# Kernel tuning notes

Measured on AMD Instinct MI355X. Metric: run time of the kernel, lower is better.

Reference implementation:

```python
import jax, jax.numpy as jnp
import numpy as np

NUM_HEAD = 8


def setup_inputs() -> dict:
    key = jax.random.key(0)
    ks = jax.random.split(key, 9)
    B, C, H, W = 4, 32, 1024, 64  # [batch, dim_input, Input_len, nodes]
    s = 1.0 / np.sqrt(C)
    return {
        "x": jax.random.normal(ks[0], (B, C, H, W), dtype=jnp.float32),
        # 1x1 conv weights stored as [out, in]
        "wq": jax.random.normal(ks[1], (C, C), dtype=jnp.float32) * s,
        "bq": jax.random.normal(ks[2], (C,), dtype=jnp.float32) * 0.01,
        "wk": jax.random.normal(ks[3], (C, C), dtype=jnp.float32) * s,
        "bk": jax.random.normal(ks[4], (C,), dtype=jnp.float32) * 0.01,
        "wv": jax.random.normal(ks[5], (C, C), dtype=jnp.float32) * s,
        "bv": jax.random.normal(ks[6], (C,), dtype=jnp.float32) * 0.01,
        # nn.Linear(num_head, 1): weight [1, num_head], bias [1]
        "w_lin": jax.random.normal(ks[7], (1, NUM_HEAD), dtype=jnp.float32) * (1.0 / np.sqrt(NUM_HEAD)),
        "b_lin": jax.random.normal(ks[8], (1,), dtype=jnp.float32) * 0.01,
    }


def reference(x, wq, bq, wk, bk, wv, bv, w_lin, b_lin):
    # x: [B, C, H, W]; 1x1 conv == channel matmul
    def conv1x1(w, b):
        return jnp.einsum("bchw,oc->bohw", x, w) + b[None, :, None, None]

    # transpose(-3,-1): [B, C, H, W] -> [B, W, H, C]
    q = conv1x1(wq, bq).transpose(0, 3, 2, 1)  # [B, W, H, C]
    k = conv1x1(wk, bk).transpose(0, 3, 2, 1)  # [B, W, H, C]
    v = conv1x1(wv, bv).transpose(0, 3, 2, 1)  # [B, W, H, C]

    H = x.shape[2]
    kd = jnp.sqrt(jnp.float32(H) / NUM_HEAD)
    scores = jnp.einsum("bwhc,bwgc->bwhg", q, k) / kd  # [B, W, H, H]
    attn = jax.nn.softmax(scores, axis=-1)
    line = jnp.einsum("bwhg,bwgc->bwhc", attn, v)  # [B, W, H, C]

    # All num_head heads share weights (dropout=identity at eval), so
    # linear1 over the stacked-head axis == line * sum(w_lin) + b_lin.
    result = line * jnp.sum(w_lin) + b_lin[0]
    # squeeze(-1) then transpose(1,3): [B, W, H, C] -> [B, C, H, W]
    return result.transpose(0, 3, 2, 1)
```

## Files before the change

### kernel.cpp

```cpp
#include <hip/hip_runtime.h>

typedef unsigned short u16;
typedef unsigned int   u32;
typedef __bf16 bf16x8 __attribute__((ext_vector_type(8)));
typedef float  f32x4  __attribute__((ext_vector_type(4)));

#define KSCALE 0.12751743f

__device__ __forceinline__ u32 cvtpk(float lo, float hi) {
    u32 r;
    asm("v_cvt_pk_bf16_f32 %0, %1, %2" : "=v"(r) : "v"(lo), "v"(hi));
    return r;
}

__global__ __launch_bounds__(256, 4) void qkv_proj(
    const float* __restrict__ x,
    const float* __restrict__ wq, const float* __restrict__ bq,
    const float* __restrict__ wk, const float* __restrict__ bk,
    const float* __restrict__ wv, const float* __restrict__ bv,
    u16* __restrict__ Qb, u16* __restrict__ Kb, u16* __restrict__ Vb)
{
    __shared__ __align__(16) u16 sW[3][32][40];
    __shared__ float sB[3][32];
    __shared__ __align__(16) u16 sO[8192];
    const int tid = threadIdx.x;
    const int b  = blockIdx.x >> 8;
    const int h0 = (blockIdx.x & 255) * 4;
    const int wid = tid >> 6, lane = tid & 63;
    const int g = lane >> 4, c = lane & 15;

    {
        const float* Ws[3] = {wq, wk, wv};
#pragma unroll
        for (int m = 0; m < 3; m++) {
            const float sc = (m == 1) ? KSCALE : 1.0f;
            for (int i = tid; i < 512; i += 256) {
                float2 v = ((const float2*)Ws[m])[i];
                int co = i >> 4, cip = i & 15;
                ((u32*)&sW[m][co][0])[cip] = cvtpk(v.x * sc, v.y * sc);
            }
        }
        if (tid < 96) {
            const float* Bs[3] = {bq, bk, bv};
            float v = Bs[tid >> 5][tid & 31];
            if ((tid >> 5) == 1) v *= KSCALE;
            ((float*)sB)[tid] = v;
        }
    }

    bf16x8 xf[4];
    {
        const float* xb = x + (size_t)b * 2097152 + (size_t)h0 * 64 + wid * 64;
#pragma unroll
        for (int pt = 0; pt < 4; pt++) {
            float f[8];
#pragma unroll
            for (int j = 0; j < 8; j++)
                f[j] = xb[(size_t)(8 * g + j) * 65536 + pt * 16 + c];
            uint4 u;
            u.x = cvtpk(f[0], f[1]); u.y = cvtpk(f[2], f[3]);
            u.z = cvtpk(f[4], f[5]); u.w = cvtpk(f[6], f[7]);
            xf[pt] = __builtin_bit_cast(bf16x8, u);
        }
    }
    __syncthreads();

    u16* outs[3] = {Qb, Kb, Vb};
    const f32x4 zz = {0.f, 0.f, 0.f, 0.f};

#pragma unroll
    for (int m = 0; m < 3; m++) {
        bf16x8 wf[2];
        float4 bias[2];
#pragma unroll
        for (int a = 0; a < 2; a++) {
            wf[a] = __builtin_bit_cast(bf16x8,
                *(const uint4*)((const char*)&sW[m][a * 16 + c][0] + g * 16));
            bias[a] = *(const float4*)&sB[m][a * 16 + g * 4];
        }

        f32x4 o[2][4];
#pragma unroll
        for (int a = 0; a < 2; a++)
#pragma unroll
            for (int pt = 0; pt < 4; pt++)
                o[a][pt] = __builtin_amdgcn_mfma_f32_16x16x32_bf16(wf[a], xf[pt], zz, 0, 0, 0);

        if (m) __syncthreads();

#pragma unroll
        for (int a = 0; a < 2; a++)
#pragma unroll
            for (int pt = 0; pt < 4; pt++) {
                int w = pt * 16 + c;
                float v0 = o[a][pt][0] + bias[a].x;
                float v1 = o[a][pt][1] + bias[a].y;
                float v2 = o[a][pt][2] + bias[a].z;
                float v3 = o[a][pt][3] + bias[a].w;
                uint2 st;
                st.x = cvtpk(v0, v1);
                st.y = cvtpk(v2, v3);
                int chunk = (wid * 4 + a * 2 + (g >> 1)) ^ (w & 7);
                *(uint2*)((char*)sO + w * 256 + chunk * 16 + (g & 1) * 8) = st;
            }
        __syncthreads();

        u16* gout = outs[m];
#pragma unroll
        for (int i = 0; i < 4; i++) {
            int L = tid + i * 256;
            int w_ = L >> 4, lc = L & 15;
            uint4 val = *(const uint4*)((const char*)sO + w_ * 256 + ((lc ^ (w_ & 7)) << 4));
            int hh = lc >> 2, sub = lc & 3;
            size_t off;
            if (m == 1) {
                int kv = h0 + hh;
                int q5 = kv & 31;
                int slot = (kv & ~31) | ((q5 & 4) << 2) | ((q5 & 24) >> 1) | (q5 & 3);
                off = (size_t)(b * 64 + w_) * 32768 + slot * 32 + (sub ^ ((slot >> 1) & 3)) * 8;
            } else {
                off = (size_t)(b * 64 + w_) * 32768 + (h0 + hh) * 32 + sub * 8;
            }
            *(uint4*)(gout + off) = val;
        }
    }
}

__global__ __launch_bounds__(1024, 2) void attn(
    const u16* __restrict__ Qb, const u16* __restrict__ Kb,
    const u16* __restrict__ Vb, float* __restrict__ Ow)
{
    __shared__ __align__(16) char sK[65536];
    __shared__ __align__(16) char sV[65536];
    const int tid = threadIdx.x;
    const int p = blockIdx.x;

    {
        const uint4* gK = (const uint4*)(Kb + (size_t)p * 32768);
        uint4* sK4 = (uint4*)sK;
        for (int m = tid; m < 4096; m += 1024)
            sK4[m] = gK[m];
        const uint4* gV = (const uint4*)(Vb + (size_t)p * 32768);
        for (int m = tid; m < 4096; m += 1024) {
            uint4 val = gV[m];
            int kv = m >> 2, c0 = (m & 3) * 8;
            const u16* pv = (const u16*)&val;
#pragma unroll
            for (int k = 0; k < 8; k++) {
                int d = c0 + k;
                int chv = (kv >> 3) ^ (d & 7) ^ ((d >> 3) & 3);
                *(u16*)(sV + d * 2048 + (chv << 4) + (kv & 7) * 2) = pv[k];
            }
        }
    }
    __syncthreads();

    const int wid = tid >> 6, lane = tid & 63;
    const int g = lane >> 4, c = lane & 15;

    bf16x8 qf[4];
    {
        const u16* qbase = Qb + (size_t)p * 32768;
#pragma unroll
        for (int nq = 0; nq < 4; nq++) {
            int row = wid * 64 + nq * 16 + c;
            qf[nq] = __builtin_bit_cast(bf16x8, *(const uint4*)(qbase + row * 32 + g * 8));
        }
    }

    bf16x8 ones;
    {
        uint4 u; u.x = u.y = u.z = u.w = 0x3F803F80u;
        ones = __builtin_bit_cast(bf16x8, u);
    }

    f32x4 o[4][2];
    f32x4 ls[4];
    const f32x4 zz = {0.f, 0.f, 0.f, 0.f};
#pragma unroll
    for (int nq = 0; nq < 4; nq++) { o[nq][0] = zz; o[nq][1] = zz; ls[nq] = zz; }

    for (int j = 0; j < 32; j++) {
        const int kv0 = j * 32;
        const int ra = kv0 + c;
        const int rb = ra + 16;
        bf16x8 k0 = __builtin_bit_cast(bf16x8,
            *(const uint4*)(sK + ra * 64 + ((g ^ ((ra >> 1) & 3)) << 4)));
        bf16x8 k1 = __builtin_bit_cast(bf16x8,
            *(const uint4*)(sK + rb * 64 + ((g ^ ((rb >> 1) & 3)) << 4)));
        const int cb = (kv0 >> 3) + g;
        bf16x8 v0 = __builtin_bit_cast(bf16x8,
            *(const uint4*)(sV + c * 2048 + ((cb ^ (c & 7) ^ ((c >> 3) & 3)) << 4)));
        bf16x8 v1 = __builtin_bit_cast(bf16x8,
            *(const uint4*)(sV + (c + 16) * 2048 + ((cb ^ (c & 7) ^ (((c + 16) >> 3) & 3)) << 4)));

        f32x4 sA[4], sB_[4];
#pragma unroll
        for (int nq = 0; nq < 4; nq++) {
            sA[nq]  = __builtin_amdgcn_mfma_f32_16x16x32_bf16(k0, qf[nq], zz, 0, 0, 0);
            sB_[nq] = __builtin_amdgcn_mfma_f32_16x16x32_bf16(k1, qf[nq], zz, 0, 0, 0);
        }
        __builtin_amdgcn_sched_barrier(0);

        bf16x8 pf[4];
#pragma unroll
        for (int nq = 0; nq < 4; nq++) {
            float p0[4], p1[4];
#pragma unroll
            for (int r = 0; r < 4; r++) {
                p0[r] = __builtin_amdgcn_exp2f(sA[nq][r]);
                p1[r] = __builtin_amdgcn_exp2f(sB_[nq][r]);
            }
            uint4 pw;
            pw.x = cvtpk(p0[0], p0[1]);
            pw.y = cvtpk(p0[2], p0[3]);
            pw.z = cvtpk(p1[0], p1[1]);
            pw.w = cvtpk(p1[2], p1[3]);
            pf[nq] = __builtin_bit_cast(bf16x8, pw);
        }
        __builtin_amdgcn_sched_barrier(0);

#pragma unroll
        for (int nq = 0; nq < 4; nq++) {
            o[nq][0] = __builtin_amdgcn_mfma_f32_16x16x32_bf16(v0, pf[nq], o[nq][0], 0, 0, 0);
            o[nq][1] = __builtin_amdgcn_mfma_f32_16x16x32_bf16(v1, pf[nq], o[nq][1], 0, 0, 0);
            ls[nq]   = __builtin_amdgcn_mfma_f32_16x16x32_bf16(ones, pf[nq], ls[nq], 0, 0, 0);
        }
    }

#pragma unroll
    for (int nq = 0; nq < 4; nq++) {
        const float inv = 1.0f / ls[nq][0];
        const int hq = wid * 64 + nq * 16 + c;
        float* dst = Ow + (size_t)p * 32768 + hq;
#pragma unroll
        for (int t = 0; t < 2; t++)
#pragma unroll
            for (int r = 0; r < 4; r++) {
                int d = t * 16 + g * 4 + r;
                dst[(size_t)d * 1024] = o[nq][t][r] * inv;
            }
    }
}

__global__ __launch_bounds__(256) void finalize_tr(
    const float* __restrict__ Ow, const float* __restrict__ w_lin,
    const float* __restrict__ b_lin, float* __restrict__ out)
{
    __shared__ float tile[64][65];
    const int tid = threadIdx.x;
    const int bi = blockIdx.x;
    const int b = bi >> 9, d = (bi >> 4) & 31, ht = bi & 15;
    const int h0 = ht * 64;

    float slin = 0.f;
#pragma unroll
    for (int i = 0; i < 8; i++) slin += w_lin[i];
    const float bl = b_lin[0];

    const int w = tid >> 2, part = tid & 3;
    const float4* src = (const float4*)(Ow + (((size_t)b * 64 + w) * 32 + d) * 1024 + h0 + part * 16);
#pragma unroll
    for (int i = 0; i < 4; i++) {
        float4 v = src[i];
        int hh = part * 16 + i * 4;
        tile[w][hh + 0] = v.x; tile[w][hh + 1] = v.y;
        tile[w][hh + 2] = v.z; tile[w][hh + 3] = v.w;
    }
    __syncthreads();

    const int ww = tid & 63, hb = tid >> 6;
    const size_t obase = ((size_t)b * 32 + d) * 1024 + h0;
#pragma unroll
    for (int k = 0; k < 16; k++) {
        int hh = k * 4 + hb;
        out[(obase + hh) * 64 + ww] = tile[ww][hh] * slin + bl;
    }
}

extern "C" void kernel_launch(void* const* d_in, const int* in_sizes, int n_in,
                              void* d_out, int out_size, void* d_ws, size_t ws_size,
                              hipStream_t stream)
{
    const float* x  = (const float*)d_in[0];
    const float* wq = (const float*)d_in[1];
    const float* bq = (const float*)d_in[2];
    const float* wk = (const float*)d_in[3];
    const float* bk = (const float*)d_in[4];
    const float* wv = (const float*)d_in[5];
    const float* bv = (const float*)d_in[6];
    const float* wl = (const float*)d_in[7];
    const float* bl = (const float*)d_in[8];
    float* out = (float*)d_out;

    char* ws = (char*)d_ws;
    u16*   Qb = (u16*)(ws);
    u16*   Kb = (u16*)(ws + (16u << 20));
    u16*   Vb = (u16*)(ws + (32u << 20));
    float* Ow = (float*)(ws + (48u << 20));

    qkv_proj<<<1024, 256, 0, stream>>>(x, wq, bq, wk, bk, wv, bv, Qb, Kb, Vb);
    attn<<<256, 1024, 0, stream>>>(Qb, Kb, Vb, Ow);
    finalize_tr<<<2048, 256, 0, stream>>>(Ow, wl, bl, out);
}
```

Measured before the change: 73.65 us.

## Software-pipeline QK^T MFMAs with softmax and store attention output as bf16

```diff
diff --git a/kernel.cpp b/kernel.cpp
--- a/kernel.cpp
+++ b/kernel.cpp
@@ -11,6 +11,9 @@
     u32 r;
     asm("v_cvt_pk_bf16_f32 %0, %1, %2" : "=v"(r) : "v"(lo), "v"(hi));
     return r;
+}
+__device__ __forceinline__ float bf2f(u32 lo16) {
+    return __builtin_bit_cast(float, lo16 << 16);
 }
 
 __global__ __launch_bounds__(256, 4) void qkv_proj(
@@ -128,7 +131,7 @@
 
 __global__ __launch_bounds__(1024, 2) void attn(
     const u16* __restrict__ Qb, const u16* __restrict__ Kb,
-    const u16* __restrict__ Vb, float* __restrict__ Ow)
+    const u16* __restrict__ Vb, u16* __restrict__ Ow)
 {
     __shared__ __align__(16) char sK[65536];
     __shared__ __align__(16) char sV[65536];
@@ -180,31 +183,48 @@
 #pragma unroll
     for (int nq = 0; nq < 4; nq++) { o[nq][0] = zz; o[nq][1] = zz; ls[nq] = zz; }
 
-    for (int j = 0; j < 32; j++) {
-        const int kv0 = j * 32;
-        const int ra = kv0 + c;
-        const int rb = ra + 16;
-        bf16x8 k0 = __builtin_bit_cast(bf16x8,
-            *(const uint4*)(sK + ra * 64 + ((g ^ ((ra >> 1) & 3)) << 4)));
-        bf16x8 k1 = __builtin_bit_cast(bf16x8,
-            *(const uint4*)(sK + rb * 64 + ((g ^ ((rb >> 1) & 3)) << 4)));
-        const int cb = (kv0 >> 3) + g;
-        bf16x8 v0 = __builtin_bit_cast(bf16x8,
-            *(const uint4*)(sV + c * 2048 + ((cb ^ (c & 7) ^ ((c >> 3) & 3)) << 4)));
-        bf16x8 v1 = __builtin_bit_cast(bf16x8,
-            *(const uint4*)(sV + (c + 16) * 2048 + ((cb ^ (c & 7) ^ (((c + 16) >> 3) & 3)) << 4)));
-
-        f32x4 sA[4], sB_[4];
+#define LOADKV(j_, K0, K1, V0, V1)                                              \
+    {                                                                           \
+        const int kv0_ = (j_) * 32;                                             \
+        const int ra_ = kv0_ + c;                                               \
+        const int rb_ = ra_ + 16;                                               \
+        K0 = __builtin_bit_cast(bf16x8,                                         \
+            *(const uint4*)(sK + ra_ * 64 + ((g ^ ((ra_ >> 1) & 3)) << 4)));    \
+        K1 = __builtin_bit_cast(bf16x8,                                         \
+            *(const uint4*)(sK + rb_ * 64 + ((g ^ ((rb_ >> 1) & 3)) << 4)));    \
+        const int cb_ = (kv0_ >> 3) + g;                                        \
+        V0 = __builtin_bit_cast(bf16x8,                                         \
+            *(const uint4*)(sV + c * 2048 + ((cb_ ^ (c & 7) ^ ((c >> 3) & 3)) << 4)));              \
+        V1 = __builtin_bit_cast(bf16x8,                                         \
+            *(const uint4*)(sV + (c + 16) * 2048 + ((cb_ ^ (c & 7) ^ (((c + 16) >> 3) & 3)) << 4)));\
+    }
+
+    f32x4 sA[4], sB_[4];
+    bf16x8 v0c, v1c;
+    {
+        bf16x8 k0, k1;
+        LOADKV(0, k0, k1, v0c, v1c);
 #pragma unroll
         for (int nq = 0; nq < 4; nq++) {
             sA[nq]  = __builtin_amdgcn_mfma_f32_16x16x32_bf16(k0, qf[nq], zz, 0, 0, 0);
             sB_[nq] = __builtin_amdgcn_mfma_f32_16x16x32_bf16(k1, qf[nq], zz, 0, 0, 0);
         }
-        __builtin_amdgcn_sched_barrier(0);
+    }
+
+    for (int j = 0; j < 32; j++) {
+        bf16x8 k0n, k1n, v0n, v1n;
+        f32x4 sAn[4] = {zz, zz, zz, zz};
+        f32x4 sBn[4] = {zz, zz, zz, zz};
+        const bool more = (j < 31);
+        if (more) LOADKV(j + 1, k0n, k1n, v0n, v1n);
 
         bf16x8 pf[4];
 #pragma unroll
         for (int nq = 0; nq < 4; nq++) {
+            if (more) {
+                sAn[nq] = __builtin_amdgcn_mfma_f32_16x16x32_bf16(k0n, qf[nq], zz, 0, 0, 0);
+                sBn[nq] = __builtin_amdgcn_mfma_f32_16x16x32_bf16(k1n, qf[nq], zz, 0, 0, 0);
+            }
             float p0[4], p1[4];
 #pragma unroll
             for (int r = 0; r < 4; r++) {
@@ -220,31 +240,39 @@
         }
         __builtin_amdgcn_sched_barrier(0);
 
+        __builtin_amdgcn_s_setprio(1);
 #pragma unroll
         for (int nq = 0; nq < 4; nq++) {
-            o[nq][0] = __builtin_amdgcn_mfma_f32_16x16x32_bf16(v0, pf[nq], o[nq][0], 0, 0, 0);
-            o[nq][1] = __builtin_amdgcn_mfma_f32_16x16x32_bf16(v1, pf[nq], o[nq][1], 0, 0, 0);
+            o[nq][0] = __builtin_amdgcn_mfma_f32_16x16x32_bf16(v0c, pf[nq], o[nq][0], 0, 0, 0);
+            o[nq][1] = __builtin_amdgcn_mfma_f32_16x16x32_bf16(v1c, pf[nq], o[nq][1], 0, 0, 0);
             ls[nq]   = __builtin_amdgcn_mfma_f32_16x16x32_bf16(ones, pf[nq], ls[nq], 0, 0, 0);
         }
-    }
+        __builtin_amdgcn_s_setprio(0);
+
+#pragma unroll
+        for (int nq = 0; nq < 4; nq++) { sA[nq] = sAn[nq]; sB_[nq] = sBn[nq]; }
+        v0c = v0n; v1c = v1n;
+    }
+#undef LOADKV
 
 #pragma unroll
     for (int nq = 0; nq < 4; nq++) {
         const float inv = 1.0f / ls[nq][0];
         const int hq = wid * 64 + nq * 16 + c;
-        float* dst = Ow + (size_t)p * 32768 + hq;
+        u16* dst = Ow + (size_t)p * 32768 + hq;
 #pragma unroll
         for (int t = 0; t < 2; t++)
 #pragma unroll
             for (int r = 0; r < 4; r++) {
                 int d = t * 16 + g * 4 + r;
-                dst[(size_t)d * 1024] = o[nq][t][r] * inv;
+                float v = o[nq][t][r] * inv;
+                dst[(size_t)d * 1024] = (u16)cvtpk(v, v);
             }
     }
 }
 
 __global__ __launch_bounds__(256) void finalize_tr(
-    const float* __restrict__ Ow, const float* __restrict__ w_lin,
+    const u16* __restrict__ Ow, const float* __restrict__ w_lin,
     const float* __restrict__ b_lin, float* __restrict__ out)
 {
     __shared__ float tile[64][65];
@@ -259,13 +287,17 @@
     const float bl = b_lin[0];
 
     const int w = tid >> 2, part = tid & 3;
-    const float4* src = (const float4*)(Ow + (((size_t)b * 64 + w) * 32 + d) * 1024 + h0 + part * 16);
-#pragma unroll
-    for (int i = 0; i < 4; i++) {
-        float4 v = src[i];
-        int hh = part * 16 + i * 4;
-        tile[w][hh + 0] = v.x; tile[w][hh + 1] = v.y;
-        tile[w][hh + 2] = v.z; tile[w][hh + 3] = v.w;
+    const u16* src = Ow + (((size_t)b * 64 + w) * 32 + d) * 1024 + h0 + part * 16;
+#pragma unroll
+    for (int i = 0; i < 2; i++) {
+        uint4 v = ((const uint4*)src)[i];
+        int hh = part * 16 + i * 8;
+        u32 a[4] = {v.x, v.y, v.z, v.w};
+#pragma unroll
+        for (int e = 0; e < 4; e++) {
+            tile[w][hh + 2 * e]     = bf2f(a[e] & 0xFFFFu);
+            tile[w][hh + 2 * e + 1] = bf2f(a[e] >> 16);
+        }
     }
     __syncthreads();
 
@@ -297,7 +329,7 @@
     u16*   Qb = (u16*)(ws);
     u16*   Kb = (u16*)(ws + (16u << 20));
     u16*   Vb = (u16*)(ws + (32u << 20));
-    float* Ow = (float*)(ws + (48u << 20));
+    u16*   Ow = (u16*)(ws + (48u << 20));
 
     qkv_proj<<<1024, 256, 0, stream>>>(x, wq, bq, wk, bk, wv, bv, Qb, Kb, Vb);
     attn<<<256, 1024, 0, stream>>>(Qb, Kb, Vb, Ow);
```

Result: slower. 104.8 us (+42.2%).

## Write V transposed from projection, split attention across two blocks, bf16 output

Applied to the files above, without the earlier changes.

```diff
diff --git a/kernel.cpp b/kernel.cpp
--- a/kernel.cpp
+++ b/kernel.cpp
@@ -11,6 +11,9 @@
     u32 r;
     asm("v_cvt_pk_bf16_f32 %0, %1, %2" : "=v"(r) : "v"(lo), "v"(hi));
     return r;
+}
+__device__ __forceinline__ float bf2f(u32 lo16) {
+    return __builtin_bit_cast(float, lo16 << 16);
 }
 
 __global__ __launch_bounds__(256, 4) void qkv_proj(
@@ -18,11 +21,12 @@
     const float* __restrict__ wq, const float* __restrict__ bq,
     const float* __restrict__ wk, const float* __restrict__ bk,
     const float* __restrict__ wv, const float* __restrict__ bv,
-    u16* __restrict__ Qb, u16* __restrict__ Kb, u16* __restrict__ Vb)
+    u16* __restrict__ Qb, u16* __restrict__ Kb, u16* __restrict__ VT)
 {
     __shared__ __align__(16) u16 sW[3][32][40];
     __shared__ float sB[3][32];
     __shared__ __align__(16) u16 sO[8192];
+    __shared__ __align__(16) u16 sVT[32][64][4];
     const int tid = threadIdx.x;
     const int b  = blockIdx.x >> 8;
     const int h0 = (blockIdx.x & 255) * 4;
@@ -65,7 +69,7 @@
     }
     __syncthreads();
 
-    u16* outs[3] = {Qb, Kb, Vb};
+    u16* outs[2] = {Qb, Kb};
     const f32x4 zz = {0.f, 0.f, 0.f, 0.f};
 
 #pragma unroll
@@ -88,70 +92,81 @@
 
         if (m) __syncthreads();
 
-#pragma unroll
-        for (int a = 0; a < 2; a++)
-#pragma unroll
-            for (int pt = 0; pt < 4; pt++) {
-                int w = pt * 16 + c;
-                float v0 = o[a][pt][0] + bias[a].x;
-                float v1 = o[a][pt][1] + bias[a].y;
-                float v2 = o[a][pt][2] + bias[a].z;
-                float v3 = o[a][pt][3] + bias[a].w;
-                uint2 st;
-                st.x = cvtpk(v0, v1);
-                st.y = cvtpk(v2, v3);
-                int chunk = (wid * 4 + a * 2 + (g >> 1)) ^ (w & 7);
-                *(uint2*)((char*)sO + w * 256 + chunk * 16 + (g & 1) * 8) = st;
-            }
-        __syncthreads();
-
-        u16* gout = outs[m];
-#pragma unroll
-        for (int i = 0; i < 4; i++) {
-            int L = tid + i * 256;
-            int w_ = L >> 4, lc = L & 15;
-            uint4 val = *(const uint4*)((const char*)sO + w_ * 256 + ((lc ^ (w_ & 7)) << 4));
-            int hh = lc >> 2, sub = lc & 3;
-            size_t off;
-            if (m == 1) {
-                int kv = h0 + hh;
-                int q5 = kv & 31;
-                int slot = (kv & ~31) | ((q5 & 4) << 2) | ((q5 & 24) >> 1) | (q5 & 3);
-                off = (size_t)(b * 64 + w_) * 32768 + slot * 32 + (sub ^ ((slot >> 1) & 3)) * 8;
-            } else {
-                off = (size_t)(b * 64 + w_) * 32768 + (h0 + hh) * 32 + sub * 8;
-            }
-            *(uint4*)(gout + off) = val;
-        }
-    }
-}
-
-__global__ __launch_bounds__(1024, 2) void attn(
-    const u16* __restrict__ Qb, const u16* __restrict__ Kb,
-    const u16* __restrict__ Vb, float* __restrict__ Ow)
+        if (m < 2) {
+#pragma unroll
+            for (int a = 0; a < 2; a++)
+#pragma unroll
+                for (int pt = 0; pt < 4; pt++) {
+                    int w = pt * 16 + c;
+                    float v0 = o[a][pt][0] + bias[a].x;
+                    float v1 = o[a][pt][1] + bias[a].y;
+                    float v2 = o[a][pt][2] + bias[a].z;
+                    float v3 = o[a][pt][3] + bias[a].w;
+                    uint2 st;
+                    st.x = cvtpk(v0, v1);
+                    st.y = cvtpk(v2, v3);
+                    int chunk = (wid * 4 + a * 2 + (g >> 1)) ^ (w & 7);
+                    *(uint2*)((char*)sO + w * 256 + chunk * 16 + (g & 1) * 8) = st;
+                }
+            __syncthreads();
+
+            u16* gout = outs[m];
+#pragma unroll
+            for (int i = 0; i < 4; i++) {
+                int L = tid + i * 256;
+                int w_ = L >> 4, lc = L & 15;
+                uint4 val = *(const uint4*)((const char*)sO + w_ * 256 + ((lc ^ (w_ & 7)) << 4));
+                int hh = lc >> 2, sub = lc & 3;
+                size_t off;
+                if (m == 1) {
+                    int kv = h0 + hh;
+                    int q5 = kv & 31;
+                    int slot = (kv & ~31) | ((q5 & 4) << 2) | ((q5 & 24) >> 1) | (q5 & 3);
+                    off = (size_t)(b * 64 + w_) * 32768 + slot * 32 + (sub ^ ((slot >> 1) & 3)) * 8;
+                } else {
+                    off = (size_t)(b * 64 + w_) * 32768 + (h0 + hh) * 32 + sub * 8;
+                }
+                *(uint4*)(gout + off) = val;
+            }
+            if (m == 1) __syncthreads();
+        } else {
+#pragma unroll
+            for (int a = 0; a < 2; a++) {
+                float bb[4] = {bias[a].x, bias[a].y, bias[a].z, bias[a].w};
+#pragma unroll
+                for (int pt = 0; pt < 4; pt++)
+#pragma unroll
+                    for (int r = 0; r < 4; r++) {
+                        float v = o[a][pt][r] + bb[r];
+                        sVT[a * 16 + g * 4 + r][pt * 16 + c][wid] = (u16)cvtpk(v, v);
+                    }
+            }
+            __syncthreads();
+#pragma unroll
+            for (int i = 0; i < 8; i++) {
+                int m_ = tid + i * 256;
+                int cc = m_ >> 6, ww = m_ & 63;
+                uint2 val = *(const uint2*)&sVT[cc][ww][0];
+                *(uint2*)(VT + (size_t)(b * 64 + ww) * 32768 + cc * 1024 + h0) = val;
+            }
+        }
+    }
+}
+
+extern "C" __global__ __attribute__((amdgpu_flat_work_group_size(512, 512), amdgpu_waves_per_eu(4, 4)))
+void attn(const u16* __restrict__ Qb, const u16* __restrict__ Kb,
+          const u16* __restrict__ VT, u16* __restrict__ Ow)
 {
     __shared__ __align__(16) char sK[65536];
-    __shared__ __align__(16) char sV[65536];
     const int tid = threadIdx.x;
-    const int p = blockIdx.x;
+    const int p  = blockIdx.x >> 1;
+    const int qh = blockIdx.x & 1;
 
     {
         const uint4* gK = (const uint4*)(Kb + (size_t)p * 32768);
         uint4* sK4 = (uint4*)sK;
-        for (int m = tid; m < 4096; m += 1024)
+        for (int m = tid; m < 4096; m += 512)
             sK4[m] = gK[m];
-        const uint4* gV = (const uint4*)(Vb + (size_t)p * 32768);
-        for (int m = tid; m < 4096; m += 1024) {
-            uint4 val = gV[m];
-            int kv = m >> 2, c0 = (m & 3) * 8;
-            const u16* pv = (const u16*)&val;
-#pragma unroll
-            for (int k = 0; k < 8; k++) {
-                int d = c0 + k;
-                int chv = (kv >> 3) ^ (d & 7) ^ ((d >> 3) & 3);
-                *(u16*)(sV + d * 2048 + (chv << 4) + (kv & 7) * 2) = pv[k];
-            }
-        }
     }
     __syncthreads();
 
@@ -160,7 +175,7 @@
 
     bf16x8 qf[4];
     {
-        const u16* qbase = Qb + (size_t)p * 32768;
+        const u16* qbase = Qb + (size_t)p * 32768 + (size_t)qh * 512 * 32;
 #pragma unroll
         for (int nq = 0; nq < 4; nq++) {
             int row = wid * 64 + nq * 16 + c;
@@ -173,6 +188,9 @@
         uint4 u; u.x = u.y = u.z = u.w = 0x3F803F80u;
         ones = __builtin_bit_cast(bf16x8, u);
     }
+
+    const u16* vt0 = VT + (size_t)p * 32768 + (size_t)c * 1024;
+    const u16* vt1 = VT + (size_t)p * 32768 + (size_t)(c + 16) * 1024;
 
     f32x4 o[4][2];
     f32x4 ls[4];
@@ -188,11 +206,6 @@
             *(const uint4*)(sK + ra * 64 + ((g ^ ((ra >> 1) & 3)) << 4)));
         bf16x8 k1 = __builtin_bit_cast(bf16x8,
             *(const uint4*)(sK + rb * 64 + ((g ^ ((rb >> 1) & 3)) << 4)));
-        const int cb = (kv0 >> 3) + g;
-        bf16x8 v0 = __builtin_bit_cast(bf16x8,
-            *(const uint4*)(sV + c * 2048 + ((cb ^ (c & 7) ^ ((c >> 3) & 3)) << 4)));
-        bf16x8 v1 = __builtin_bit_cast(bf16x8,
-            *(const uint4*)(sV + (c + 16) * 2048 + ((cb ^ (c & 7) ^ (((c + 16) >> 3) & 3)) << 4)));
 
         f32x4 sA[4], sB_[4];
 #pragma unroll
@@ -202,6 +215,8 @@
         }
         __builtin_amdgcn_sched_barrier(0);
 
+        bf16x8 v0 = __builtin_bit_cast(bf16x8, *(const uint4*)(vt0 + kv0 + g * 8));
+        bf16x8 v1 = __builtin_bit_cast(bf16x8, *(const uint4*)(vt1 + kv0 + g * 8));
         bf16x8 pf[4];
 #pragma unroll
         for (int nq = 0; nq < 4; nq++) {
@@ -220,31 +235,34 @@
         }
         __builtin_amdgcn_sched_barrier(0);
 
+        __builtin_amdgcn_s_setprio(1);
 #pragma unroll
         for (int nq = 0; nq < 4; nq++) {
             o[nq][0] = __builtin_amdgcn_mfma_f32_16x16x32_bf16(v0, pf[nq], o[nq][0], 0, 0, 0);
             o[nq][1] = __builtin_amdgcn_mfma_f32_16x16x32_bf16(v1, pf[nq], o[nq][1], 0, 0, 0);
             ls[nq]   = __builtin_amdgcn_mfma_f32_16x16x32_bf16(ones, pf[nq], ls[nq], 0, 0, 0);
         }
+        __builtin_amdgcn_s_setprio(0);
     }
 
 #pragma unroll
     for (int nq = 0; nq < 4; nq++) {
         const float inv = 1.0f / ls[nq][0];
-        const int hq = wid * 64 + nq * 16 + c;
-        float* dst = Ow + (size_t)p * 32768 + hq;
+        const int hq = qh * 512 + wid * 64 + nq * 16 + c;
+        u16* dst = Ow + (size_t)p * 32768 + hq;
 #pragma unroll
         for (int t = 0; t < 2; t++)
 #pragma unroll
             for (int r = 0; r < 4; r++) {
                 int d = t * 16 + g * 4 + r;
-                dst[(size_t)d * 1024] = o[nq][t][r] * inv;
+                float v = o[nq][t][r] * inv;
+                dst[(size_t)d * 1024] = (u16)cvtpk(v, v);
             }
     }
 }
 
 __global__ __launch_bounds__(256) void finalize_tr(
-    const float* __restrict__ Ow, const float* __restrict__ w_lin,
+    const u16* __restrict__ Ow, const float* __restrict__ w_lin,
     const float* __restrict__ b_lin, float* __restrict__ out)
 {
     __shared__ float tile[64][65];
@@ -259,13 +277,17 @@
     const float bl = b_lin[0];
 
     const int w = tid >> 2, part = tid & 3;
-    const float4* src = (const float4*)(Ow + (((size_t)b * 64 + w) * 32 + d) * 1024 + h0 + part * 16);
-#pragma unroll
-    for (int i = 0; i < 4; i++) {
-        float4 v = src[i];
-        int hh = part * 16 + i * 4;
-        tile[w][hh + 0] = v.x; tile[w][hh + 1] = v.y;
-        tile[w][hh + 2] = v.z; tile[w][hh + 3] = v.w;
+    const u16* src = Ow + (((size_t)b * 64 + w) * 32 + d) * 1024 + h0 + part * 16;
+#pragma unroll
+    for (int i = 0; i < 2; i++) {
+        uint4 v = ((const uint4*)src)[i];
+        int hh = part * 16 + i * 8;
+        u32 a[4] = {v.x, v.y, v.z, v.w};
+#pragma unroll
+        for (int e = 0; e < 4; e++) {
+            tile[w][hh + 2 * e]     = bf2f(a[e] & 0xFFFFu);
+            tile[w][hh + 2 * e + 1] = bf2f(a[e] >> 16);
+        }
     }
     __syncthreads();
 
@@ -296,10 +318,10 @@
     char* ws = (char*)d_ws;
     u16*   Qb = (u16*)(ws);
     u16*   Kb = (u16*)(ws + (16u << 20));
-    u16*   Vb = (u16*)(ws + (32u << 20));
-    float* Ow = (float*)(ws + (48u << 20));
-
-    qkv_proj<<<1024, 256, 0, stream>>>(x, wq, bq, wk, bk, wv, bv, Qb, Kb, Vb);
-    attn<<<256, 1024, 0, stream>>>(Qb, Kb, Vb, Ow);
+    u16*   VT = (u16*)(ws + (32u << 20));
+    u16*   Ow = (u16*)(ws + (48u << 20));
+
+    qkv_proj<<<1024, 256, 0, stream>>>(x, wq, bq, wk, bk, wv, bv, Qb, Kb, VT);
+    attn<<<512, 512, 0, stream>>>(Qb, Kb, VT, Ow);
     finalize_tr<<<2048, 256, 0, stream>>>(Ow, wl, bl, out);
 }
```

Result: slower. 92.95 us (+26.2%).
